# Optimization experiments

Measured on AMD Instinct MI355X. Metric: run time of the kernel, lower is better.

## Reference

```python
import jax, jax.numpy as jnp
import numpy as np

TAU_PRE = 2.0   # pre-synaptic trace time constant
SCALE = 1.0     # forward(scale=1.0) default
SPIKE_P = 0.1   # firing probability for realistic binary spike trains


def setup_inputs() -> dict:
    key = jax.random.key(0)
    k1, k2 = jax.random.split(key)
    T, B, NIN, NOUT = 2048, 128, 256, 128
    # binary spike trains, [T, B, N]
    in_spikes = (jax.random.uniform(k1, (T, B, NIN)) < SPIKE_P).astype(jnp.float32)
    out_spikes = (jax.random.uniform(k2, (T, B, NOUT)) < SPIKE_P).astype(jnp.float32)
    return {"in_spikes": in_spikes, "out_spikes": out_spikes}


def reference(in_spikes, out_spikes):
    # STDP.forward: loop over recorded timesteps, per step:
    #   trace_pre = trace_pre - trace_pre/tau_pre + in_spike          (decayed trace)
    #   dw = sum_b trace_pre[b, :] (outer) out_spike[b, :] -> [NOUT, NIN]
    #   delta_w += scale * dw
    # Expressed as a single lax.scan over the time axis.
    B, NIN = in_spikes.shape[1], in_spikes.shape[2]
    NOUT = out_spikes.shape[2]

    def step(carry, xs):
        trace_pre, delta_w = carry
        s_in, s_out = xs                                 # [B, NIN], [B, NOUT]
        trace_pre = trace_pre - trace_pre / TAU_PRE + s_in
        dw = jnp.einsum('bi,bo->oi', trace_pre, s_out)   # [NOUT, NIN]
        return (trace_pre, delta_w + SCALE * dw), None

    init = (jnp.zeros((B, NIN), in_spikes.dtype),
            jnp.zeros((NOUT, NIN), in_spikes.dtype))
    (_, delta_w), _ = jax.lax.scan(step, init, (in_spikes, out_spikes))
    return delta_w
```

## Files before the change

kernel.cpp:

```cpp
#include <hip/hip_runtime.h>
#include <hip/hip_bf16.h>

#define T_TOTAL 2048
#define BATCH   128
#define NIN     256
#define NOUT    128

#define TC      256
#define BC      4
#define WARM    32
#define G       4
#define NTC     (T_TOTAL / TC)
#define NBC     (BATCH / BC)
#define NBLOCKS (NTC * NBC)
#define NG      (TC / G)

#define OUT_ELEMS (NOUT * NIN)

static_assert(NG % 2 == 0, "2-stage pipeline needs even group count");

typedef __attribute__((ext_vector_type(8)))  __bf16 bf16x8;
typedef __attribute__((ext_vector_type(2)))  __bf16 bf16x2;
typedef __attribute__((ext_vector_type(16))) float  f32x16;

static __device__ __forceinline__ unsigned pack_bf16(float a, float b) {
    bf16x2 v = { (__bf16)a, (__bf16)b };
    union { bf16x2 v; unsigned u; } c; c.v = v; return c.u;
}

static __device__ __forceinline__ bf16x8 frag_from4(unsigned d0, unsigned d1,
                                                    unsigned d2, unsigned d3) {
    union { unsigned u[4]; bf16x8 v; } c;
    c.u[0] = d0; c.u[1] = d1; c.u[2] = d2; c.u[3] = d3; return c.v;
}

static __device__ __forceinline__ void gload16(const float* g, void* l) {
    __builtin_amdgcn_global_load_lds(
        (const __attribute__((address_space(1))) void*)g,
        (__attribute__((address_space(3))) void*)l,
        16, 0, 0);
}

__global__ __launch_bounds__(512, 2)
void stdp_main(const float* __restrict__ in, const float* __restrict__ outs,
               float* __restrict__ dst, int nslots, int use_atomic)
{
    __shared__ float in_lds [2][G * BC * NIN];
    __shared__ float out_lds[2][G * BC * NOUT];

    const int tid = threadIdx.x;
    const int bc  = blockIdx.x % NBC;
    const int tc  = blockIdx.x / NBC;
    const int b0  = bc * BC;
    const int t0  = tc * TC;

    const int lane = tid & 63;
    const int wv   = tid >> 6;
    const int mt   = wv & 3;
    const int nh   = wv >> 2;
    const int l31  = lane & 31;
    const int kh   = lane >> 5;

    const size_t OST = (size_t)BATCH * NOUT;

    const float* __restrict__ outW = outs + (size_t)(b0 + 2 * kh) * NOUT + mt * 32 + l31;
    float rtrA = 0.f, rtrB = 0.f;
    if (tc < NTC - 1) {
        for (int tb = t0 + TC + WARM; tb > t0 + TC; tb -= 8) {
            float vA[8], vB[8];
#pragma unroll
            for (int u = 0; u < 8; ++u) {
                vA[u] = outW[(size_t)(tb - 1 - u) * OST];
                vB[u] = outW[(size_t)(tb - 1 - u) * OST + NOUT];
            }
#pragma unroll
            for (int u = 0; u < 8; ++u) {
                rtrA = vA[u] + 0.5f * rtrA;
                rtrB = vB[u] + 0.5f * rtrB;
            }
        }
    }

    f32x16 acc[4];
#pragma unroll
    for (int j = 0; j < 4; ++j) acc[j] = (f32x16)(0.f);

    const float* inS  = in   + (size_t)(b0 + (wv & 3)) * NIN  + lane * 4;
    const float* outS = outs + (size_t)(b0 + 2 * (wv & 1) + kh) * NOUT + l31 * 4;
    const int    tin  = wv >> 2;
    const int    tot  = wv >> 1;
    char* inL  = (char*)&in_lds[0][0]  + wv * 1024;
    char* outL = (char*)&out_lds[0][0] + wv * 1024;

    auto dma_group = [&](int s, int g) {
        const int tg = t0 + g * G;
        gload16(inS  + (size_t)(tg + tin)     * (BATCH * NIN),  inL + s * 16384);
        gload16(inS  + (size_t)(tg + tin + 2) * (BATCH * NIN),  inL + s * 16384 + 8192);
        gload16(outS + (size_t)(tg + tot)     * (BATCH * NOUT), outL + s * 8192);
    };

    const char* ilb = (const char*)&in_lds [0][0] + kh * 2048 + nh * 512 + l31 * 4;
    const char* olb = (const char*)&out_lds[0][0] + kh * 1024 + mt * 128 + l31 * 4;

    auto body = [&](int s, int g, int vm) {
        if (vm) asm volatile("s_waitcnt vmcnt(3)" ::: "memory");
        else    asm volatile("s_waitcnt vmcnt(0)" ::: "memory");
        __builtin_amdgcn_s_barrier();
        __builtin_amdgcn_sched_barrier(0);

        float vA[4], vB[4];
#pragma unroll
        for (int q = 0; q < 4; ++q) {
            vA[q] = *(const float*)(olb + s * 8192 + q * 2048);
            vB[q] = *(const float*)(olb + s * 8192 + q * 2048 + 512);
        }
        float aA[4], aB[4];
#pragma unroll
        for (int q = 3; q >= 0; --q) {
            rtrA = vA[q] + 0.5f * rtrA; aA[q] = rtrA;
            rtrB = vB[q] + 0.5f * rtrB; aB[q] = rtrB;
        }
        const bf16x8 a = frag_from4(pack_bf16(aA[0], aA[1]), pack_bf16(aA[2], aA[3]),
                                    pack_bf16(aB[0], aB[1]), pack_bf16(aB[2], aB[3]));
        bf16x8 bfr[4];
#pragma unroll
        for (int tn = 0; tn < 4; ++tn) {
            float p[8];
#pragma unroll
            for (int be = 0; be < 2; ++be)
#pragma unroll
                for (int q = 0; q < 4; ++q)
                    p[be * 4 + q] = *(const float*)
                        (ilb + s * 16384 + q * 4096 + be * 1024 + tn * 128);
            bfr[tn] = frag_from4(pack_bf16(p[0], p[1]), pack_bf16(p[2], p[3]),
                                 pack_bf16(p[4], p[5]), pack_bf16(p[6], p[7]));
        }
#pragma unroll
        for (int tn = 0; tn < 4; ++tn)
            acc[tn] = __builtin_amdgcn_mfma_f32_32x32x16_bf16(a, bfr[tn], acc[tn], 0, 0, 0);

        asm volatile("s_waitcnt lgkmcnt(0)" ::: "memory");
        __builtin_amdgcn_s_barrier();
        __builtin_amdgcn_sched_barrier(0);
        if (g >= 2) dma_group(s, g - 2);
    };

    dma_group(1, NG - 1);
    dma_group(0, NG - 2);
    for (int gg = NG - 1; gg >= 3; gg -= 2) {
        body(1, gg, 1);
        body(0, gg - 1, 1);
    }
    body(1, 1, 1);
    body(0, 0, 0);

    float* base = dst + (size_t)(use_atomic ? (blockIdx.x % nslots) : blockIdx.x) * OUT_ELEMS;
#pragma unroll
    for (int j = 0; j < 4; ++j) {
        const int icol = (nh * 4 + j) * 32 + l31;
#pragma unroll
        for (int r = 0; r < 16; ++r) {
            const int row = (r & 3) + 8 * (r >> 2) + 4 * kh;
            const int o   = mt * 32 + row;
            const float v = acc[j][r];
            if (use_atomic) atomicAdd(&base[o * NIN + icol], v);
            else            base[o * NIN + icol] = v;
        }
    }
}

__global__ void zero_kernel(float* p, int n) {
    int i = blockIdx.x * blockDim.x + threadIdx.x;
    if (i < n) p[i] = 0.f;
}

__global__ __launch_bounds__(256)
void reduce_kernel(const float* __restrict__ ws, float* __restrict__ outp, int nslots) {
    const int idx = blockIdx.x * 256 + threadIdx.x;
    float s = 0.f;
    int k = 0;
    for (; k + 16 <= nslots; k += 16) {
        float v[16];
#pragma unroll
        for (int u = 0; u < 16; ++u) v[u] = ws[(size_t)(k + u) * OUT_ELEMS + idx];
#pragma unroll
        for (int u = 0; u < 16; ++u) s += v[u];
    }
    for (; k < nslots; ++k) s += ws[(size_t)k * OUT_ELEMS + idx];
    outp[idx] = s;
}

extern "C" void kernel_launch(void* const* d_in, const int* in_sizes, int n_in,
                              void* d_out, int out_size, void* d_ws, size_t ws_size,
                              hipStream_t stream) {
    const float* in   = (const float*)d_in[0];
    const float* outs = (const float*)d_in[1];
    float* out = (float*)d_out;
    float* ws  = (float*)d_ws;

    const size_t slot_bytes = (size_t)OUT_ELEMS * sizeof(float);

    if (ws_size >= (size_t)NBLOCKS * slot_bytes) {
        stdp_main<<<NBLOCKS, 512, 0, stream>>>(in, outs, ws, NBLOCKS, 0);
        reduce_kernel<<<OUT_ELEMS / 256, 256, 0, stream>>>(ws, out, NBLOCKS);
    } else if (ws_size >= 16 * slot_bytes) {
        zero_kernel<<<(16 * OUT_ELEMS + 255) / 256, 256, 0, stream>>>(ws, 16 * OUT_ELEMS);
        stdp_main<<<NBLOCKS, 512, 0, stream>>>(in, outs, ws, 16, 1);
        reduce_kernel<<<OUT_ELEMS / 256, 256, 0, stream>>>(ws, out, 16);
    } else {
        zero_kernel<<<(OUT_ELEMS + 255) / 256, 256, 0, stream>>>(out, OUT_ELEMS);
        stdp_main<<<NBLOCKS, 512, 0, stream>>>(in, outs, out, 1, 1);
    }
}
```

Before: 442.8 us.

## Deepen input DMA pipeline to four stages and load out-spikes directly to registers

```diff
diff --git a/kernel.cpp b/kernel.cpp
--- a/kernel.cpp
+++ b/kernel.cpp
@@ -17,7 +17,7 @@
 
 #define OUT_ELEMS (NOUT * NIN)
 
-static_assert(NG % 2 == 0, "2-stage pipeline needs even group count");
+static_assert(NG % 4 == 0, "4-stage pipeline needs NG % 4 == 0");
 
 typedef __attribute__((ext_vector_type(8)))  __bf16 bf16x8;
 typedef __attribute__((ext_vector_type(2)))  __bf16 bf16x2;
@@ -41,12 +41,19 @@
         16, 0, 0);
 }
 
+static __device__ __forceinline__ void wait_vm(int N) {
+    if      (N == 12) asm volatile("s_waitcnt vmcnt(12)" ::: "memory");
+    else if (N == 10) asm volatile("s_waitcnt vmcnt(10)" ::: "memory");
+    else if (N == 8)  asm volatile("s_waitcnt vmcnt(8)"  ::: "memory");
+    else if (N == 6)  asm volatile("s_waitcnt vmcnt(6)"  ::: "memory");
+    else              asm volatile("s_waitcnt vmcnt(0)"  ::: "memory");
+}
+
 __global__ __launch_bounds__(512, 2)
 void stdp_main(const float* __restrict__ in, const float* __restrict__ outs,
                float* __restrict__ dst, int nslots, int use_atomic)
 {
-    __shared__ float in_lds [2][G * BC * NIN];
-    __shared__ float out_lds[2][G * BC * NOUT];
+    __shared__ float in_lds[4][G * BC * NIN];
 
     const int tid = threadIdx.x;
     const int bc  = blockIdx.x % NBC;
@@ -62,9 +69,10 @@
     const int kh   = lane >> 5;
 
     const size_t OST = (size_t)BATCH * NOUT;
-
     const float* __restrict__ outW = outs + (size_t)(b0 + 2 * kh) * NOUT + mt * 32 + l31;
+
     float rtrA = 0.f, rtrB = 0.f;
+
     if (tc < NTC - 1) {
         for (int tb = t0 + TC + WARM; tb > t0 + TC; tb -= 8) {
             float vA[8], vB[8];
@@ -85,40 +93,38 @@
 #pragma unroll
     for (int j = 0; j < 4; ++j) acc[j] = (f32x16)(0.f);
 
-    const float* inS  = in   + (size_t)(b0 + (wv & 3)) * NIN  + lane * 4;
-    const float* outS = outs + (size_t)(b0 + 2 * (wv & 1) + kh) * NOUT + l31 * 4;
-    const int    tin  = wv >> 2;
-    const int    tot  = wv >> 1;
-    char* inL  = (char*)&in_lds[0][0]  + wv * 1024;
-    char* outL = (char*)&out_lds[0][0] + wv * 1024;
-
-    auto dma_group = [&](int s, int g) {
+    const float* inS = in + (size_t)(b0 + (wv & 3)) * NIN + lane * 4;
+    const int    tin = wv >> 2;
+    char* inL = (char*)&in_lds[0][0] + wv * 1024;
+
+    auto dma_in = [&](int s, int g) {
         const int tg = t0 + g * G;
-        gload16(inS  + (size_t)(tg + tin)     * (BATCH * NIN),  inL + s * 16384);
-        gload16(inS  + (size_t)(tg + tin + 2) * (BATCH * NIN),  inL + s * 16384 + 8192);
-        gload16(outS + (size_t)(tg + tot)     * (BATCH * NOUT), outL + s * 8192);
+        gload16(inS + (size_t)(tg + tin)     * (BATCH * NIN), inL + s * 16384);
+        gload16(inS + (size_t)(tg + tin + 2) * (BATCH * NIN), inL + s * 16384 + 8192);
     };
 
-    const char* ilb = (const char*)&in_lds [0][0] + kh * 2048 + nh * 512 + l31 * 4;
-    const char* olb = (const char*)&out_lds[0][0] + kh * 1024 + mt * 128 + l31 * 4;
-
-    auto body = [&](int s, int g, int vm) {
-        if (vm) asm volatile("s_waitcnt vmcnt(3)" ::: "memory");
-        else    asm volatile("s_waitcnt vmcnt(0)" ::: "memory");
+    float OA0[8], OA1[8];
+    auto oload = [&](float (&A)[8], int g) {
+        const int tg = t0 + g * G;
+#pragma unroll
+        for (int q = 0; q < 4; ++q) {
+            A[q]     = outW[(size_t)(tg + q) * OST];
+            A[4 + q] = outW[(size_t)(tg + q) * OST + NOUT];
+        }
+    };
+
+    const char* ilb = (const char*)&in_lds[0][0] + kh * 2048 + nh * 512 + l31 * 4;
+
+    auto body = [&](int s, const float (&A)[8], int N) {
+        wait_vm(N);
         __builtin_amdgcn_s_barrier();
         __builtin_amdgcn_sched_barrier(0);
 
-        float vA[4], vB[4];
-#pragma unroll
-        for (int q = 0; q < 4; ++q) {
-            vA[q] = *(const float*)(olb + s * 8192 + q * 2048);
-            vB[q] = *(const float*)(olb + s * 8192 + q * 2048 + 512);
-        }
         float aA[4], aB[4];
 #pragma unroll
         for (int q = 3; q >= 0; --q) {
-            rtrA = vA[q] + 0.5f * rtrA; aA[q] = rtrA;
-            rtrB = vB[q] + 0.5f * rtrB; aB[q] = rtrB;
+            rtrA = A[q]     + 0.5f * rtrA; aA[q] = rtrA;
+            rtrB = A[4 + q] + 0.5f * rtrB; aB[q] = rtrB;
         }
         const bf16x8 a = frag_from4(pack_bf16(aA[0], aA[1]), pack_bf16(aA[2], aA[3]),
                                     pack_bf16(aB[0], aB[1]), pack_bf16(aB[2], aB[3]));
@@ -142,17 +148,41 @@
         asm volatile("s_waitcnt lgkmcnt(0)" ::: "memory");
         __builtin_amdgcn_s_barrier();
         __builtin_amdgcn_sched_barrier(0);
-        if (g >= 2) dma_group(s, g - 2);
     };
 
-    dma_group(1, NG - 1);
-    dma_group(0, NG - 2);
-    for (int gg = NG - 1; gg >= 3; gg -= 2) {
-        body(1, gg, 1);
-        body(0, gg - 1, 1);
-    }
-    body(1, 1, 1);
-    body(0, 0, 0);
+#define SLOT(S, GG, BANK, N)                                   \
+    do {                                                       \
+        body(S, BANK, N);                                      \
+        if ((GG) >= 2) oload(BANK, (GG) - 2);                  \
+        __builtin_amdgcn_sched_barrier(0);                     \
+        if ((GG) >= 4) dma_in(S, (GG) - 4);                    \
+        __builtin_amdgcn_sched_barrier(0);                     \
+    } while (0)
+
+    oload(OA1, NG - 1);
+    oload(OA0, NG - 2);
+    __builtin_amdgcn_sched_barrier(0);
+    dma_in(3, NG - 1);
+    dma_in(2, NG - 2);
+    dma_in(1, NG - 3);
+    dma_in(0, NG - 4);
+    __builtin_amdgcn_sched_barrier(0);
+
+    SLOT(3, NG - 1, OA1, 6);
+    SLOT(2, NG - 2, OA0, 12);
+    SLOT(1, NG - 3, OA1, 12);
+    SLOT(0, NG - 4, OA0, 12);
+    for (int gg = NG - 5; gg >= 7; gg -= 4) {
+        SLOT(3, gg,     OA1, 12);
+        SLOT(2, gg - 1, OA0, 12);
+        SLOT(1, gg - 2, OA1, 12);
+        SLOT(0, gg - 3, OA0, 12);
+    }
+    SLOT(3, 3, OA1, 12);
+    SLOT(2, 2, OA0, 10);
+    SLOT(1, 1, OA1, 8);
+    SLOT(0, 0, OA0, 0);
+#undef SLOT
 
     float* base = dst + (size_t)(use_atomic ? (blockIdx.x % nslots) : blockIdx.x) * OUT_ELEMS;
 #pragma unroll
```

New measurement: 443.6 us. About the same (+0.2%).
